# Kernel optimization log

Measured on AMD Instinct MI355X. Metric: run time of the kernel, lower is better.

## Reference

```python
import jax, jax.numpy as jnp
import numpy as np

B, V, CIN, COUT, TDIM = 2, 65536, 128, 256, 512
EPS = 1e-5
G1, G2 = 32, 32  # _gn_num_groups(128)=32, _gn_num_groups(256)=32


def group_norm(x, w, b, groups):
    # x: [B, V, C]; torch GroupNorm on [B, C, V] normalizes per (batch, group)
    # over the group's channels AND all V positions (biased variance).
    Bx, Vx, C = x.shape
    xr = x.reshape(Bx, Vx, groups, C // groups)
    mean = xr.mean(axis=(1, 3), keepdims=True)
    var = xr.var(axis=(1, 3), keepdims=True)
    xn = ((xr - mean) * jax.lax.rsqrt(var + EPS)).reshape(Bx, Vx, C)
    return xn * w + b


def neigh_conv(x, neigh, W, b):
    # x: [B, V, C]; neigh: [V, 9]; W: [out, 9*C]; b: [out]
    C = x.shape[-1]
    gathered = x[:, neigh]                      # [B, V, 9, C]
    Wr = W.reshape(-1, 9, C)                    # [out, 9, C]
    return jnp.einsum('bvnc,onc->bvo', gathered, Wr) + b


def setup_inputs() -> dict:
    key = jax.random.key(0)
    ks = jax.random.split(key, 12)
    s = 0.02
    return {
        'x': jax.random.normal(ks[0], (B, V, CIN), jnp.float32),
        't_emb': jax.random.normal(ks[1], (B, TDIM), jnp.float32),
        'neigh_orders': jax.random.randint(ks[2], (V, 9), 0, V, jnp.int64)
            if jax.config.jax_enable_x64 else jax.random.randint(ks[2], (V, 9), 0, V, jnp.int32),
        'gn1_w': jnp.ones((CIN,), jnp.float32),
        'gn1_b': jnp.zeros((CIN,), jnp.float32),
        'w1': jax.random.normal(ks[3], (COUT, 9 * CIN), jnp.float32) * s,
        'b1': jnp.zeros((COUT,), jnp.float32),
        'wt': jax.random.normal(ks[4], (COUT, TDIM), jnp.float32) * s,
        'bt': jnp.zeros((COUT,), jnp.float32),
        'gn2_w': jnp.ones((COUT,), jnp.float32),
        'gn2_b': jnp.zeros((COUT,), jnp.float32),
        'w2': jax.random.normal(ks[5], (COUT, 9 * COUT), jnp.float32) * s,
        'b2': jnp.zeros((COUT,), jnp.float32),
        'ws': jax.random.normal(ks[6], (COUT, CIN), jnp.float32) * s,
        'bs': jnp.zeros((COUT,), jnp.float32),
    }


def reference(x, t_emb, neigh_orders, gn1_w, gn1_b, w1, b1, wt, bt,
              gn2_w, gn2_b, w2, b2, ws, bs):
    h = group_norm(x, gn1_w, gn1_b, G1)
    h = jax.nn.silu(h)
    h = neigh_conv(h, neigh_orders, w1, b1)                 # [B, V, COUT]
    t = jax.nn.silu(t_emb) @ wt.T + bt                      # [B, COUT]
    h = h + t[:, None, :]
    h = group_norm(h, gn2_w, gn2_b, G2)
    h = jax.nn.silu(h)
    h = neigh_conv(h, neigh_orders, w2, b2)                 # [B, V, COUT]
    shortcut = x @ ws.T + bs                                # learned 1x1 (in_ch != out_ch)
    return h + shortcut
```

## Files before the change

kernel.cpp:

```cpp
#include <hip/hip_runtime.h>
#include <hip/hip_bf16.h>

#define DEV __device__ __forceinline__

typedef __attribute__((ext_vector_type(8))) short bf16x8;
typedef __attribute__((ext_vector_type(4))) float f32x4;

constexpr int Bb = 2, V = 65536, CIN = 128, COUT = 256, TDIM = 512;
constexpr float EPS = 1e-5f;
constexpr int K1 = 1152, K2 = 2304, K2e = 2432;
constexpr int NCH1 = 128;
constexpr int NCH2 = 256;
constexpr int W1N = (K1/8)*COUT*8;
constexpr int W2N = (K2e/8)*COUT*8;

DEV float silu_f(float x){ return x / (1.f + __expf(-x)); }
DEV unsigned short f2b(float x){
  union { float f; unsigned u; } v; v.f = x;
  unsigned r = v.u + 0x7fffu + ((v.u >> 16) & 1u);
  return (unsigned short)(r >> 16);
}
DEV float b2f(unsigned short h){ union { unsigned u; float f; } v; v.u = ((unsigned)h) << 16; return v.f; }

__global__ void k_gn1_partial(const float* __restrict__ x, float* __restrict__ part){
  int b = blockIdx.y, ch = blockIdx.x;
  int t = threadIdx.x;
  int c = t & 127;
  int r0 = t >> 7;
  float s = 0.f, ss = 0.f;
  const float* xp = x + ((size_t)b*V + (size_t)ch*512)*CIN + c;
  for (int r = r0; r < 512; r += 2){
    float v = xp[(size_t)r*CIN];
    s += v; ss += v*v;
  }
  __shared__ float s_s[256], s_q[256];
  s_s[t] = s; s_q[t] = ss; __syncthreads();
  if (t < 128){ s_s[t] += s_s[t+128]; s_q[t] += s_q[t+128]; }
  __syncthreads();
  if (t < 32){
    float a = 0, q = 0;
    for (int i = 0; i < 4; ++i){ a += s_s[t*4+i]; q += s_q[t*4+i]; }
    int idx = ((b*32 + t)*NCH1 + ch)*2;
    part[idx] = a; part[idx+1] = q;
  }
}

__global__ void k_gn1_final(const float* __restrict__ part, const float* __restrict__ w,
                            const float* __restrict__ bias, float* __restrict__ sc,
                            float* __restrict__ bi){
  int t = threadIdx.x;
  if (t >= Bb*32) return;
  float s = 0, q = 0;
  for (int ch = 0; ch < NCH1; ++ch){ s += part[(t*NCH1+ch)*2]; q += part[(t*NCH1+ch)*2+1]; }
  float n = (float)V * 4.f;
  float mean = s / n;
  float var = q / n - mean*mean;
  float inv = rsqrtf(var + EPS);
  int b = t >> 5, g = t & 31;
  for (int j = 0; j < 4; ++j){
    int c = g*4 + j;
    float scl = w[c] * inv;
    sc[b*CIN + c] = scl;
    bi[b*CIN + c] = bias[c] - mean*scl;
  }
}

__global__ void k_act1(const float* __restrict__ x, const float* __restrict__ sc,
                       const float* __restrict__ bi, unsigned short* __restrict__ act1,
                       unsigned short* __restrict__ xb){
  size_t i = ((size_t)blockIdx.x*256 + threadIdx.x)*4;
  int c = (int)(i & (CIN-1));
  int b = (int)(i >> 23);
  float4 v = *(const float4*)(x + i);
  const float* scp = sc + b*CIN + c;
  const float* bip = bi + b*CIN + c;
  ushort4 a, xo;
  a.x = f2b(silu_f(v.x*scp[0] + bip[0]));
  a.y = f2b(silu_f(v.y*scp[1] + bip[1]));
  a.z = f2b(silu_f(v.z*scp[2] + bip[2]));
  a.w = f2b(silu_f(v.w*scp[3] + bip[3]));
  xo.x = f2b(v.x); xo.y = f2b(v.y); xo.z = f2b(v.z); xo.w = f2b(v.w);
  *(ushort4*)(act1 + i) = a;
  *(ushort4*)(xb + i)   = xo;
}

__global__ void k_prepW(const float* __restrict__ w1, const float* __restrict__ w2,
                        const float* __restrict__ wsm, unsigned short* __restrict__ W1b,
                        unsigned short* __restrict__ W2b){
  int i = blockIdx.x*256 + threadIdx.x;
  if (i < W1N){
    int j = i & 7, o = (i >> 3) & 255, k8 = i >> 11;
    W1b[i] = f2b(w1[o*K1 + k8*8 + j]);
  }
  int i2 = i - W1N;
  if (i2 >= 0 && i2 < W2N){
    int j = i2 & 7, o = (i2 >> 3) & 255, k8 = i2 >> 11;
    int k = k8*8 + j;
    float v = (k < K2) ? w2[o*K2 + k] : wsm[o*CIN + (k - K2)];
    W2b[i2] = f2b(v);
  }
}

__global__ void k_tcomb(const float* __restrict__ temb, const float* __restrict__ wt,
                        const float* __restrict__ bt, const float* __restrict__ b1,
                        float* __restrict__ tc){
  int b = blockIdx.y;
  int o = blockIdx.x*4 + (threadIdx.x >> 6);
  int l = threadIdx.x & 63;
  const float* tb = temb + (size_t)b*TDIM;
  const float* wr = wt + (size_t)o*TDIM;
  float acc = 0.f;
  #pragma unroll
  for (int k = l; k < TDIM; k += 64)
    acc += silu_f(tb[k]) * wr[k];
  #pragma unroll
  for (int off = 32; off > 0; off >>= 1) acc += __shfl_down(acc, off, 64);
  if (l == 0) tc[b*COUT + o] = acc + bt[o] + b1[o];
}

template<int CINR, int NCHUNK, int CPN, bool CONV2>
__launch_bounds__(256)
__global__ void k_conv(const unsigned short* __restrict__ act,
                       const unsigned short* __restrict__ xb,
                       const unsigned short* __restrict__ Wb,
                       const int* __restrict__ neigh,
                       const float* __restrict__ tc,
                       const float* __restrict__ b2,
                       const float* __restrict__ bs,
                       unsigned short* __restrict__ outb,
                       float* __restrict__ outf){
  __shared__ __align__(16) unsigned short A_lds[2][128*64];
  __shared__ __align__(16) unsigned short B_lds[2][64*128];
  __shared__ int nb[128*9];
  const int tid = threadIdx.x;
  const int w = tid >> 6, lane = tid & 63;
  const int d = blockIdx.x;
  const int bx = ((d >> 4) << 3) + (d & 7);
  const int n0 = ((d >> 3) & 1) << 7;
  const int vflat = bx << 7;
  const int b = vflat >> 16;
  const int vb = vflat & (V-1);
  for (int i = tid; i < 128*9; i += 256) nb[i] = neigh[(size_t)vb*9 + i];

  f32x4 acc[4][4] = {};
  const int wm = w >> 1, wn = w & 1;
  const int quad = lane >> 4, l15 = lane & 15;
  const int sr = lane >> 3, ssg = lane & 7;

  const unsigned short* actb = act + (size_t)b*V*CINR;
  const unsigned short* xbb  = CONV2 ? (xb + (size_t)b*V*CIN) : (const unsigned short*)nullptr;

  auto STAGE = [&](int chunk, int buf){
    {
      int nidx = 0, c0, rl;
      const unsigned short* src;
      const bool scseg = CONV2 && (chunk >= NCHUNK-2);
      if (scseg){ c0 = (chunk - (NCHUNK-2))*64; src = xbb; rl = CIN; }
      else      { nidx = chunk / CPN; c0 = (chunk % CPN)*64; src = actb; rl = CINR; }
      #pragma unroll
      for (int i = 0; i < 4; ++i){
        int row  = (w<<5) + (i<<3) + sr;
        int rowg = scseg ? (vb + row) : nb[row*9 + nidx];
        int g = ssg ^ (row & 7);
        const unsigned short* gp = src + (size_t)rowg*rl + c0 + g*8;
        unsigned short* lp = &A_lds[buf][((w<<5) + (i<<3))<<6];
        __builtin_amdgcn_global_load_lds(gp, lp, 16, 0, 0);
      }
    }
    {
      const unsigned short* wsrc = Wb + (size_t)chunk*8*COUT*8;
      #pragma unroll
      for (int i = 0; i < 4; ++i){
        int e = (w<<2) + i;
        int q8 = e >> 1, nh = e & 1;
        const unsigned short* gp = wsrc + ((size_t)q8*COUT + n0 + (nh<<6) + lane)*8;
        unsigned short* lp = &B_lds[buf][q8*1024 + (nh<<9)];
        __builtin_amdgcn_global_load_lds(gp, lp, 16, 0, 0);
      }
    }
  };

  auto COMPUTE = [&](int cur){
    __builtin_amdgcn_s_setprio(1);
    #pragma unroll
    for (int ks = 0; ks < 2; ++ks){
      bf16x8 av[4], bv[4];
      #pragma unroll
      for (int mt = 0; mt < 4; ++mt){
        int m = (wm<<6) + (mt<<4) + l15;
        int seg = ((ks<<2) + quad) ^ (l15 & 7);
        av[mt] = *(const bf16x8*)&A_lds[cur][(m<<6) + (seg<<3)];
      }
      #pragma unroll
      for (int nt = 0; nt < 4; ++nt){
        int n = (wn<<6) + (nt<<4) + l15;
        bv[nt] = *(const bf16x8*)&B_lds[cur][(((ks<<2)+quad)<<10) + (n<<3)];
      }
      #pragma unroll
      for (int mt = 0; mt < 4; ++mt)
        #pragma unroll
        for (int nt = 0; nt < 4; ++nt)
          acc[mt][nt] = __builtin_amdgcn_mfma_f32_16x16x32_bf16(av[mt], bv[nt], acc[mt][nt], 0, 0, 0);
    }
    __builtin_amdgcn_s_setprio(0);
  };

  __syncthreads();
  STAGE(0, 0);

  #pragma unroll 2
  for (int chunk = 0; chunk < NCHUNK-1; ++chunk){
    const int cur = chunk & 1;
    STAGE(chunk + 1, cur ^ 1);
    asm volatile("s_waitcnt vmcnt(8)" ::: "memory");
    __builtin_amdgcn_s_barrier();
    asm volatile("" ::: "memory");
    COMPUTE(cur);
    asm volatile("" ::: "memory");
    __builtin_amdgcn_s_barrier();
    asm volatile("" ::: "memory");
  }
  asm volatile("s_waitcnt vmcnt(0)" ::: "memory");
  __builtin_amdgcn_s_barrier();
  asm volatile("" ::: "memory");
  COMPUTE((NCHUNK-1) & 1);

  #pragma unroll
  for (int mt = 0; mt < 4; ++mt){
    #pragma unroll
    for (int nt = 0; nt < 4; ++nt){
      int col = n0 + (wn<<6) + (nt<<4) + l15;
      float bval = CONV2 ? (b2[col] + bs[col]) : tc[b*COUT + col];
      #pragma unroll
      for (int rg = 0; rg < 4; ++rg){
        int row = (wm<<6) + (mt<<4) + (quad<<2) + rg;
        size_t off = ((size_t)(vflat + row))*COUT + col;
        float v = acc[mt][nt][rg] + bval;
        if (CONV2) outf[off] = v;
        else       outb[off] = f2b(v);
      }
    }
  }
}

__global__ void k_gn2_partial(const unsigned short* __restrict__ h1, float* __restrict__ part){
  int b = blockIdx.y, ch = blockIdx.x;
  int t = threadIdx.x;
  float s = 0.f, ss = 0.f;
  const unsigned short* p = h1 + ((size_t)b*V + (size_t)ch*256)*COUT + t;
  for (int r = 0; r < 256; ++r){
    float v = b2f(p[(size_t)r*COUT]);
    s += v; ss += v*v;
  }
  __shared__ float s_s[256], s_q[256];
  s_s[t] = s; s_q[t] = ss; __syncthreads();
  if (t < 32){
    float a = 0, q = 0;
    for (int i = 0; i < 8; ++i){ a += s_s[t*8+i]; q += s_q[t*8+i]; }
    int idx = ((b*32 + t)*NCH2 + ch)*2;
    part[idx] = a; part[idx+1] = q;
  }
}

__global__ void k_gn2_final(const float* __restrict__ part, const float* __restrict__ w,
                            const float* __restrict__ bias, float* __restrict__ sc,
                            float* __restrict__ bi){
  int t = threadIdx.x;
  if (t >= Bb*32) return;
  float s = 0, q = 0;
  for (int ch = 0; ch < NCH2; ++ch){ s += part[(t*NCH2+ch)*2]; q += part[(t*NCH2+ch)*2+1]; }
  float n = (float)V * 8.f;
  float mean = s / n, var = q / n - mean*mean, inv = rsqrtf(var + EPS);
  int b = t >> 5, g = t & 31;
  for (int j = 0; j < 8; ++j){
    int c = g*8 + j;
    float scl = w[c] * inv;
    sc[b*COUT + c] = scl;
    bi[b*COUT + c] = bias[c] - mean*scl;
  }
}

__global__ void k_act2(unsigned short* __restrict__ h1, const float* __restrict__ sc,
                       const float* __restrict__ bi){
  size_t i = ((size_t)blockIdx.x*256 + threadIdx.x)*4;
  int c = (int)(i & (COUT-1));
  int b = (int)(i >> 24);
  ushort4 h = *(ushort4*)(h1 + i);
  const float* scp = sc + b*COUT + c;
  const float* bip = bi + b*COUT + c;
  ushort4 o;
  o.x = f2b(silu_f(b2f(h.x)*scp[0] + bip[0]));
  o.y = f2b(silu_f(b2f(h.y)*scp[1] + bip[1]));
  o.z = f2b(silu_f(b2f(h.z)*scp[2] + bip[2]));
  o.w = f2b(silu_f(b2f(h.w)*scp[3] + bip[3]));
  *(ushort4*)(h1 + i) = o;
}

extern "C" void kernel_launch(void* const* d_in, const int* in_sizes, int n_in,
                              void* d_out, int out_size, void* d_ws, size_t ws_size,
                              hipStream_t stream){
  const float* x    = (const float*)d_in[0];
  const float* temb = (const float*)d_in[1];
  const int*   neigh= (const int*)d_in[2];
  const float* gn1w = (const float*)d_in[3];
  const float* gn1b = (const float*)d_in[4];
  const float* w1   = (const float*)d_in[5];
  const float* b1   = (const float*)d_in[6];
  const float* wt   = (const float*)d_in[7];
  const float* bt   = (const float*)d_in[8];
  const float* gn2w = (const float*)d_in[9];
  const float* gn2b = (const float*)d_in[10];
  const float* w2   = (const float*)d_in[11];
  const float* b2   = (const float*)d_in[12];
  const float* wsm  = (const float*)d_in[13];
  const float* bs   = (const float*)d_in[14];
  float* out = (float*)d_out;

  char* wsp = (char*)d_ws;
  unsigned short* act1 = (unsigned short*)(wsp);
  unsigned short* xb   = (unsigned short*)(wsp + 33554432);
  unsigned short* h1   = (unsigned short*)(wsp + 67108864);
  unsigned short* W1b  = (unsigned short*)(wsp + 134217728);
  unsigned short* W2b  = (unsigned short*)(wsp + 134217728 + 589824);
  char* p = wsp + 134217728 + 589824 + 1245184;
  float* tc    = (float*)p;  p += 2048;
  float* part1 = (float*)p;  p += (size_t)Bb*32*NCH1*2*4;
  float* part2 = (float*)p;  p += (size_t)Bb*32*NCH2*2*4;
  float* sc1   = (float*)p;  p += 1024;
  float* bi1   = (float*)p;  p += 1024;
  float* sc2   = (float*)p;  p += 2048;
  float* bi2   = (float*)p;  p += 2048;

  k_gn1_partial<<<dim3(NCH1, Bb), 256, 0, stream>>>(x, part1);
  k_gn1_final  <<<1, 64, 0, stream>>>(part1, gn1w, gn1b, sc1, bi1);
  k_act1       <<<16384, 256, 0, stream>>>(x, sc1, bi1, act1, xb);
  k_prepW      <<<(W1N + W2N)/256, 256, 0, stream>>>(w1, w2, wsm, W1b, W2b);
  k_tcomb      <<<dim3(COUT/4, Bb), 256, 0, stream>>>(temb, wt, bt, b1, tc);
  k_conv<128, 18, 2, false><<<2048, 256, 0, stream>>>(act1, nullptr, W1b, neigh, tc, nullptr, nullptr, h1, nullptr);
  k_gn2_partial<<<dim3(NCH2, Bb), 256, 0, stream>>>(h1, part2);
  k_gn2_final  <<<1, 64, 0, stream>>>(part2, gn2w, gn2b, sc2, bi2);
  k_act2       <<<32768, 256, 0, stream>>>(h1, sc2, bi2);
  k_conv<256, 38, 4, true><<<2048, 256, 0, stream>>>(h1, xb, W2b, neigh, nullptr, b2, bs, nullptr, out);
}
```

Before: 629.2 us.

## Load conv operands straight into registers, double-buffered, instead of via LDS

Removes the LDS staging buffers and the barrier-synchronised pipeline in the gathered-neighbour conv GEMM. Each wave now loads its own A rows (gathered activations) and B columns (weights) from global memory directly into MFMA operand registers, with two register sets alternating across chunks. Launch bounds now request two blocks per CU. This gets rid of LDS writes and reads and the block-wide barriers, but each A and B tile is now fetched by two waves, doubling global/L2 traffic. It also adds register pressure and leaves gather latency less hidden.

New measurement: 867.7 us. 1.38x slower.

```diff
diff --git a/kernel.cpp b/kernel.cpp
--- a/kernel.cpp
+++ b/kernel.cpp
@@ -119,7 +119,7 @@
 }
 
 template<int CINR, int NCHUNK, int CPN, bool CONV2>
-__launch_bounds__(256)
+__launch_bounds__(256, 2)
 __global__ void k_conv(const unsigned short* __restrict__ act,
                        const unsigned short* __restrict__ xb,
                        const unsigned short* __restrict__ Wb,
@@ -129,8 +129,6 @@
                        const float* __restrict__ bs,
                        unsigned short* __restrict__ outb,
                        float* __restrict__ outf){
-  __shared__ __align__(16) unsigned short A_lds[2][128*64];
-  __shared__ __align__(16) unsigned short B_lds[2][64*128];
   __shared__ int nb[128*9];
   const int tid = threadIdx.x;
   const int w = tid >> 6, lane = tid & 63;
@@ -145,85 +143,54 @@
   f32x4 acc[4][4] = {};
   const int wm = w >> 1, wn = w & 1;
   const int quad = lane >> 4, l15 = lane & 15;
-  const int sr = lane >> 3, ssg = lane & 7;
 
   const unsigned short* actb = act + (size_t)b*V*CINR;
   const unsigned short* xbb  = CONV2 ? (xb + (size_t)b*V*CIN) : (const unsigned short*)nullptr;
-
-  auto STAGE = [&](int chunk, int buf){
-    {
-      int nidx = 0, c0, rl;
-      const unsigned short* src;
-      const bool scseg = CONV2 && (chunk >= NCHUNK-2);
-      if (scseg){ c0 = (chunk - (NCHUNK-2))*64; src = xbb; rl = CIN; }
-      else      { nidx = chunk / CPN; c0 = (chunk % CPN)*64; src = actb; rl = CINR; }
-      #pragma unroll
-      for (int i = 0; i < 4; ++i){
-        int row  = (w<<5) + (i<<3) + sr;
-        int rowg = scseg ? (vb + row) : nb[row*9 + nidx];
-        int g = ssg ^ (row & 7);
-        const unsigned short* gp = src + (size_t)rowg*rl + c0 + g*8;
-        unsigned short* lp = &A_lds[buf][((w<<5) + (i<<3))<<6];
-        __builtin_amdgcn_global_load_lds(gp, lp, 16, 0, 0);
-      }
+  const unsigned short* wq = Wb + (size_t)quad*COUT*8 + (size_t)(n0 + (wn<<6) + l15)*8;
+
+  __syncthreads();
+
+  auto ISSUE = [&](int chunk, bf16x8 (&av)[8], bf16x8 (&bv)[8]){
+    const bool scseg = CONV2 && (chunk >= NCHUNK-2);
+    int nidx = 0, c0, rl;
+    const unsigned short* src;
+    if (scseg){ c0 = (chunk - (NCHUNK-2))*64; src = xbb; rl = CIN; }
+    else      { nidx = chunk / CPN; c0 = (chunk % CPN)*64; src = actb; rl = CINR; }
+    #pragma unroll
+    for (int mt = 0; mt < 4; ++mt){
+      int row = (wm<<6) + (mt<<4) + l15;
+      int rowg = scseg ? (vb + row) : nb[row*9 + nidx];
+      const unsigned short* rp = src + (size_t)rowg*rl + c0 + (quad<<3);
+      av[mt*2+0] = *(const bf16x8*)(rp);
+      av[mt*2+1] = *(const bf16x8*)(rp + 32);
     }
-    {
-      const unsigned short* wsrc = Wb + (size_t)chunk*8*COUT*8;
-      #pragma unroll
-      for (int i = 0; i < 4; ++i){
-        int e = (w<<2) + i;
-        int q8 = e >> 1, nh = e & 1;
-        const unsigned short* gp = wsrc + ((size_t)q8*COUT + n0 + (nh<<6) + lane)*8;
-        unsigned short* lp = &B_lds[buf][q8*1024 + (nh<<9)];
-        __builtin_amdgcn_global_load_lds(gp, lp, 16, 0, 0);
-      }
+    const unsigned short* wp = wq + (size_t)chunk*8*COUT*8;
+    #pragma unroll
+    for (int nt = 0; nt < 4; ++nt){
+      bv[nt*2+0] = *(const bf16x8*)(wp + (nt<<7));
+      bv[nt*2+1] = *(const bf16x8*)(wp + 4*COUT*8 + (nt<<7));
     }
   };
 
-  auto COMPUTE = [&](int cur){
-    __builtin_amdgcn_s_setprio(1);
+  auto COMP = [&](bf16x8 (&av)[8], bf16x8 (&bv)[8]){
     #pragma unroll
-    for (int ks = 0; ks < 2; ++ks){
-      bf16x8 av[4], bv[4];
-      #pragma unroll
-      for (int mt = 0; mt < 4; ++mt){
-        int m = (wm<<6) + (mt<<4) + l15;
-        int seg = ((ks<<2) + quad) ^ (l15 & 7);
-        av[mt] = *(const bf16x8*)&A_lds[cur][(m<<6) + (seg<<3)];
-      }
-      #pragma unroll
-      for (int nt = 0; nt < 4; ++nt){
-        int n = (wn<<6) + (nt<<4) + l15;
-        bv[nt] = *(const bf16x8*)&B_lds[cur][(((ks<<2)+quad)<<10) + (n<<3)];
-      }
+    for (int ks = 0; ks < 2; ++ks)
       #pragma unroll
       for (int mt = 0; mt < 4; ++mt)
         #pragma unroll
         for (int nt = 0; nt < 4; ++nt)
-          acc[mt][nt] = __builtin_amdgcn_mfma_f32_16x16x32_bf16(av[mt], bv[nt], acc[mt][nt], 0, 0, 0);
-    }
-    __builtin_amdgcn_s_setprio(0);
+          acc[mt][nt] = __builtin_amdgcn_mfma_f32_16x16x32_bf16(av[mt*2+ks], bv[nt*2+ks], acc[mt][nt], 0, 0, 0);
   };
 
-  __syncthreads();
-  STAGE(0, 0);
-
-  #pragma unroll 2
-  for (int chunk = 0; chunk < NCHUNK-1; ++chunk){
-    const int cur = chunk & 1;
-    STAGE(chunk + 1, cur ^ 1);
-    asm volatile("s_waitcnt vmcnt(8)" ::: "memory");
-    __builtin_amdgcn_s_barrier();
-    asm volatile("" ::: "memory");
-    COMPUTE(cur);
-    asm volatile("" ::: "memory");
-    __builtin_amdgcn_s_barrier();
-    asm volatile("" ::: "memory");
-  }
-  asm volatile("s_waitcnt vmcnt(0)" ::: "memory");
-  __builtin_amdgcn_s_barrier();
-  asm volatile("" ::: "memory");
-  COMPUTE((NCHUNK-1) & 1);
+  bf16x8 a0[8], b0[8], a1[8], b1[8];
+  ISSUE(0, a0, b0);
+  #pragma unroll 1
+  for (int c = 0; c < NCHUNK; c += 2){
+    ISSUE(c+1, a1, b1);
+    COMP(a0, b0);
+    if (c+2 < NCHUNK) ISSUE(c+2, a0, b0);
+    COMP(a1, b1);
+  }
 
   #pragma unroll
   for (int mt = 0; mt < 4; ++mt){
```
